# Kernel optimization log

Measured on AMD Instinct MI355X. Metric: run time of the kernel, lower is better.

The kernel has to match this reference:

```python
import jax, jax.numpy as jnp
import numpy as np

FEAT = 256
HID = FEAT // 2
N_KEYS = 2          # output_keys = ["energy_0", "energy_1"]
N_MOLS = 2000
ATOMS_PER_MOL = 100
N_ATOMS = N_MOLS * ATOMS_PER_MOL
LOG2 = 0.6931471805599453


def shifted_softplus(x):
    # NFF's shifted softplus: softplus(x) - log(2)
    return jax.nn.softplus(x) - LOG2


def setup_inputs() -> dict:
    key = jax.random.key(0)
    ks = jax.random.split(key, 6)
    s_i = jax.random.normal(ks[0], (N_ATOMS, FEAT), dtype=jnp.float32)
    xyz = jax.random.normal(ks[1], (N_ATOMS, 3), dtype=jnp.float32)
    num_atoms = jnp.full((N_MOLS,), ATOMS_PER_MOL, dtype=jnp.int64)
    # Per-key MLP params stacked over keys: Linear(F->H), act, Linear(H->1)
    W1 = jax.random.normal(ks[2], (N_KEYS, FEAT, HID), dtype=jnp.float32) / np.sqrt(FEAT)
    b1 = jnp.zeros((N_KEYS, HID), dtype=jnp.float32)
    W2 = jax.random.normal(ks[3], (N_KEYS, HID), dtype=jnp.float32) / np.sqrt(HID)
    b2 = jnp.zeros((N_KEYS,), dtype=jnp.float32)
    return {"s_i": s_i, "xyz": xyz, "num_atoms": num_atoms,
            "W1": W1, "b1": b1, "W2": W2, "b2": b2}


def reference(s_i, xyz, num_atoms, W1, b1, W2, b2):
    n_mols = num_atoms.shape[0]
    # segment id per atom, replacing the torch.split(...)+per-chunk sum loop
    seg = jnp.repeat(jnp.arange(n_mols), num_atoms,
                     total_repeat_length=s_i.shape[0])        # [N]
    # per-key MLP: [K,N,H] hidden, [K,N] scalar output per atom
    h = shifted_softplus(jnp.einsum('nf,kfh->knh', s_i, W1) + b1[:, None, :])
    val = jnp.einsum('knh,kh->kn', h, W2) + b2[:, None]       # [K, N]
    # fused segment-sum pooling -> per-molecule scalars
    pooled = jax.ops.segment_sum(val.T, seg, num_segments=n_mols)  # [M, K]
    return pooled.T                                            # [K, M]
```

## Files before the change

### kernel.cpp

```cpp
#include <hip/hip_runtime.h>

#define FEAT 256
#define HID 128
#define NKEYS 2

typedef __bf16 bf16x8 __attribute__((ext_vector_type(8)));
typedef float f32x16 __attribute__((ext_vector_type(16)));

union Frag {
    bf16x8 v;
    unsigned u[4];
    uint4 q;
};

__device__ __forceinline__ unsigned pack_bf16_2(float f0, float f1) {
    unsigned u0 = __float_as_uint(f0) + 0x8000u;
    unsigned u1 = __float_as_uint(f1) + 0x8000u;
    return __builtin_amdgcn_perm(u1, u0, 0x07060302u);
}

__device__ __forceinline__ float ssp(float x) {
    float sp = __logf(1.0f + __expf(x));
    sp = (x > 15.0f) ? x : sp;
    return sp - 0.69314718056f;
}

__device__ __forceinline__ int find_mol(const int* off, int n_mols, int g) {
    int lo = 0, hi = n_mols;
    while (hi - lo > 1) {
        int mid = (lo + hi) >> 1;
        if (off[mid] <= g) lo = mid; else hi = mid;
    }
    return lo;
}

__device__ __forceinline__ void gload_lds16(const float* g, void* l) {
    __builtin_amdgcn_global_load_lds(
        (const __attribute__((address_space(1))) unsigned int*)g,
        (__attribute__((address_space(3))) unsigned int*)l,
        16, 0, 0);
}

__global__ void prep_kernel(const void* __restrict__ num_atoms_raw,
                            const float* __restrict__ W1,
                            int n_mols, int n_atoms,
                            int* __restrict__ off,
                            unsigned short* __restrict__ Bp,
                            float* __restrict__ out, int out_n) {
    if (blockIdx.x > 0) {
        int idx = (blockIdx.x - 1) * 256 + threadIdx.x;
        int c = idx >> 8;
        int k = idx & 255;
        int key = c >> 7, j = c & 127;
        float f = W1[(size_t)key * FEAT * HID + (size_t)k * HID + j];
        unsigned u = __float_as_uint(f);
        unsigned r = (u + 0x7FFFu + ((u >> 16) & 1u)) >> 16;
        Bp[(size_t)c * FEAT + k] = (unsigned short)r;
        return;
    }
    for (int i = threadIdx.x; i < out_n; i += 256) out[i] = 0.0f;

    __shared__ long long tsum[256];
    __shared__ int csum[256];
    int tid = threadIdx.x;
    const int* a32 = (const int*)num_atoms_raw;
    const long long* a64 = (const long long*)num_atoms_raw;
    int chunk = (n_mols + 255) >> 8;
    int lo = tid * chunk;
    if (lo > n_mols) lo = n_mols;
    int hi = lo + chunk;
    if (hi > n_mols) hi = n_mols;

    long long s32 = 0;
    for (int i = lo; i < hi; ++i) s32 += (long long)a32[i];
    tsum[tid] = s32;
    __syncthreads();
    #pragma unroll
    for (int d = 128; d > 0; d >>= 1) {
        if (tid < d) tsum[tid] += tsum[tid + d];
        __syncthreads();
    }
    int mode = (tsum[0] == (long long)n_atoms) ? 0 : 1;
    long long s = s32;
    if (mode) {
        s = 0;
        for (int i = lo; i < hi; ++i) s += a64[i];
    }
    int v = (int)s;
    csum[tid] = v;
    __syncthreads();
    #pragma unroll
    for (int d = 1; d < 256; d <<= 1) {
        int t = (tid >= d) ? csum[tid - d] : 0;
        __syncthreads();
        csum[tid] += t;
        __syncthreads();
    }
    int run = csum[tid] - v;
    for (int i = lo; i < hi; ++i) {
        off[i] = run;
        run += mode ? (int)a64[i] : a32[i];
    }
    if (hi >= n_mols) off[n_mols] = run;
}

__global__ __launch_bounds__(256, 2)
void gemm_fused(const float* __restrict__ A,
                const unsigned short* __restrict__ Bp,
                const float* __restrict__ b1,
                const float* __restrict__ W2,
                const float* __restrict__ b2,
                const int* __restrict__ off,
                float* __restrict__ out,
                int n_atoms, int n_mols) {
    __shared__ uint4 ldsA[4096];
    int*   offlds = (int*)ldsA;
    float (*part)[64] = (float(*)[64])((char*)ldsA + 8192);
    float (*molacc)[4] = (float(*)[4])((char*)ldsA + 9216);
    int*   mol0sh = (int*)((char*)ldsA + 9248);

    const int tid  = threadIdx.x;
    const int lane = tid & 63;
    const int wid  = tid >> 6;
    const int l31  = lane & 31;
    const int half = lane >> 5;
    const int m0   = blockIdx.x * 64;

    const bool lds_off_ok = (n_mols + 1) <= 2048;
    int4 ov0, ov1;
    if (lds_off_ok) {
        const int4* o4 = (const int4*)off;
        ov0 = o4[tid * 2];
        ov1 = o4[tid * 2 + 1];
    }

    #pragma unroll
    for (int i = 0; i < 4; ++i) {
        const int p   = i * 256 + wid * 64 + lane;
        const int row = p >> 4;
        const int u   = (p & 15) ^ (row & 15);
        int gr = m0 + row;
        if (gr > n_atoms - 1) gr = n_atoms - 1;
        const float* g = A + (size_t)gr * FEAT + u * 4;
        #pragma unroll
        for (int c = 0; c < 4; ++c) {
            gload_lds16(g + c * 64, (void*)&ldsA[c * 1024 + i * 256 + wid * 64]);
        }
    }

    const int c0 = wid * 64 + l31;
    const unsigned short* bb0 = Bp + (size_t)c0 * FEAT + half * 8;
    const unsigned short* bb1 = Bp + (size_t)(c0 + 32) * FEAT + half * 8;
    const int s = l31 & 15;
    const float b1c0 = b1[c0], b1c1 = b1[c0 + 32];
    const float w2c0 = W2[c0], w2c1 = W2[c0 + 32];

    __syncthreads();

    f32x16 acc00 = 0.0f, acc01 = 0.0f, acc10 = 0.0f, acc11 = 0.0f;

    #pragma unroll
    for (int c = 0; c < 4; ++c) {
        const uint4* lbuf = ldsA + c * 1024;
        const int kb = c * 64;
        Frag bf0[4], bf1[4];
        #pragma unroll
        for (int j = 0; j < 4; ++j) {
            bf0[j].q = *(const uint4*)(bb0 + kb + j * 16);
            bf1[j].q = *(const uint4*)(bb1 + kb + j * 16);
        }
        #pragma unroll
        for (int j = 0; j < 4; ++j) {
            const int u0 = j * 4 + half * 2;
            const int q0 = u0 ^ s;
            const int base0 = l31 * 16;
            const int base1 = (l31 + 32) * 16;
            uint4 lo0 = lbuf[base0 + q0];
            uint4 hi0 = lbuf[base0 + (q0 ^ 1)];
            uint4 lo1 = lbuf[base1 + q0];
            uint4 hi1 = lbuf[base1 + (q0 ^ 1)];
            const float4 fl0 = *(const float4*)&lo0;
            const float4 fh0 = *(const float4*)&hi0;
            const float4 fl1 = *(const float4*)&lo1;
            const float4 fh1 = *(const float4*)&hi1;
            Frag a0, a1;
            a0.u[0] = pack_bf16_2(fl0.x, fl0.y);
            a0.u[1] = pack_bf16_2(fl0.z, fl0.w);
            a0.u[2] = pack_bf16_2(fh0.x, fh0.y);
            a0.u[3] = pack_bf16_2(fh0.z, fh0.w);
            a1.u[0] = pack_bf16_2(fl1.x, fl1.y);
            a1.u[1] = pack_bf16_2(fl1.z, fl1.w);
            a1.u[2] = pack_bf16_2(fh1.x, fh1.y);
            a1.u[3] = pack_bf16_2(fh1.z, fh1.w);
            acc00 = __builtin_amdgcn_mfma_f32_32x32x16_bf16(a0.v, bf0[j].v, acc00, 0, 0, 0);
            acc01 = __builtin_amdgcn_mfma_f32_32x32x16_bf16(a0.v, bf1[j].v, acc01, 0, 0, 0);
            acc10 = __builtin_amdgcn_mfma_f32_32x32x16_bf16(a1.v, bf0[j].v, acc10, 0, 0, 0);
            acc11 = __builtin_amdgcn_mfma_f32_32x32x16_bf16(a1.v, bf1[j].v, acc11, 0, 0, 0);
        }
    }

    __syncthreads();

    if (lds_off_ok) {
        ((int4*)offlds)[tid * 2]     = ov0;
        ((int4*)offlds)[tid * 2 + 1] = ov1;
    }
    if (tid < NKEYS * 4) molacc[tid >> 2][tid & 3] = 0.0f;

    #pragma unroll
    for (int rt = 0; rt < 2; ++rt) {
        const f32x16& Ac0 = rt ? acc10 : acc00;
        const f32x16& Ac1 = rt ? acc11 : acc01;
        #pragma unroll
        for (int r = 0; r < 16; ++r) {
            float t = ssp(Ac0[r] + b1c0) * w2c0 + ssp(Ac1[r] + b1c1) * w2c1;
            t += __shfl_xor(t, 1);
            t += __shfl_xor(t, 2);
            t += __shfl_xor(t, 4);
            t += __shfl_xor(t, 8);
            t += __shfl_xor(t, 16);
            if (l31 == r) {
                int row = rt * 32 + (r & 3) + 8 * (r >> 2) + 4 * half;
                part[wid][row] = t;
            }
        }
    }
    __syncthreads();

    if (tid < NKEYS * 64) {
        int key = tid >> 6, r = tid & 63;
        int gm = m0 + r;
        const int* o = lds_off_ok ? offlds : off;
        int mol0 = find_mol(o, n_mols, m0);
        if (tid == 0) *mol0sh = mol0;
        if (gm < n_atoms) {
            int mol = find_mol(o, n_mols, gm);
            float val = part[2 * key][r] + part[2 * key + 1][r] + b2[key];
            int ml = mol - mol0;
            if (ml < 4) atomicAdd(&molacc[key][ml], val);
            else        atomicAdd(&out[(size_t)key * n_mols + mol], val);
        }
    }
    __syncthreads();

    if (tid < NKEYS * 4) {
        int key = tid >> 2, ml = tid & 3;
        int mol = *mol0sh + ml;
        if (mol < n_mols) {
            float v = molacc[key][ml];
            if (v != 0.0f) atomicAdd(&out[(size_t)key * n_mols + mol], v);
        }
    }
}

extern "C" void kernel_launch(void* const* d_in, const int* in_sizes, int n_in,
                              void* d_out, int out_size, void* d_ws, size_t ws_size,
                              hipStream_t stream) {
    const float* s_i      = (const float*)d_in[0];
    const void*  num_atoms = d_in[2];
    const float* W1 = (const float*)d_in[3];
    const float* b1 = (const float*)d_in[4];
    const float* W2 = (const float*)d_in[5];
    const float* b2 = (const float*)d_in[6];
    int n_atoms = in_sizes[0] / FEAT;
    int n_mols  = in_sizes[2];
    float* out = (float*)d_out;

    int* off = (int*)d_ws;
    size_t off_bytes = (((size_t)(n_mols + 1) * 4) + 255) & ~(size_t)255;
    unsigned short* Bp = (unsigned short*)((char*)d_ws + off_bytes);

    int pack_blocks = (NKEYS * HID * FEAT) / 256;
    prep_kernel<<<1 + pack_blocks, 256, 0, stream>>>(num_atoms, W1, n_mols, n_atoms,
                                                     off, Bp, out, out_size);

    int gblocks = (n_atoms + 63) / 64;
    gemm_fused<<<gblocks, 256, 0, stream>>>(s_i, Bp, b1, W2, b2, off, out, n_atoms, n_mols);
}
```

Before: 389.0 us.

## Make fused GEMM persistent with double-buffered LDS staging across tiles

Replaces the one-block-per-64-row-tile launch with a persistent grid of at most 512 blocks of 512 threads. Each block loops over tiles and double-buffers 64-column A chunks in LDS, so the global loads for the next chunk or tile overlap the MFMA work on the current one. Each wave now owns 32 hidden columns instead of 64, which halves the accumulator registers. Molecule lookup and the flush of partial molecule sums are deferred by one tile. In exchange the kernel takes a barrier per K chunk and has more complex cross-tile bookkeeping.

```diff
diff --git a/kernel.cpp b/kernel.cpp
--- a/kernel.cpp
+++ b/kernel.cpp
@@ -104,7 +104,7 @@
     if (hi >= n_mols) off[n_mols] = run;
 }
 
-__global__ __launch_bounds__(256, 2)
+__global__ __launch_bounds__(512, 4)
 void gemm_fused(const float* __restrict__ A,
                 const unsigned short* __restrict__ Bp,
                 const float* __restrict__ b1,
@@ -112,143 +112,165 @@
                 const float* __restrict__ b2,
                 const int* __restrict__ off,
                 float* __restrict__ out,
-                int n_atoms, int n_mols) {
-    __shared__ uint4 ldsA[4096];
-    int*   offlds = (int*)ldsA;
-    float (*part)[64] = (float(*)[64])((char*)ldsA + 8192);
-    float (*molacc)[4] = (float(*)[4])((char*)ldsA + 9216);
-    int*   mol0sh = (int*)((char*)ldsA + 9248);
+                int n_atoms, int n_mols, int ntiles, int stride) {
+    __shared__ uint4  ldsA[2][1024];
+    __shared__ int    offlds[2048];
+    __shared__ float  part[2][8][64];
+    __shared__ int    rowmol[2][64];
+    __shared__ float  molacc[2][NKEYS][4];
 
     const int tid  = threadIdx.x;
     const int lane = tid & 63;
     const int wid  = tid >> 6;
     const int l31  = lane & 31;
     const int half = lane >> 5;
-    const int m0   = blockIdx.x * 64;
-
-    const bool lds_off_ok = (n_mols + 1) <= 2048;
-    int4 ov0, ov1;
-    if (lds_off_ok) {
-        const int4* o4 = (const int4*)off;
-        ov0 = o4[tid * 2];
-        ov1 = o4[tid * 2 + 1];
-    }
-
-    #pragma unroll
-    for (int i = 0; i < 4; ++i) {
-        const int p   = i * 256 + wid * 64 + lane;
-        const int row = p >> 4;
-        const int u   = (p & 15) ^ (row & 15);
-        int gr = m0 + row;
-        if (gr > n_atoms - 1) gr = n_atoms - 1;
-        const float* g = A + (size_t)gr * FEAT + u * 4;
+
+    const bool lds_ok = (n_mols + 1) <= 2048;
+    if (lds_ok) ((int4*)offlds)[tid] = ((const int4*)off)[tid];
+    if (tid < 2 * NKEYS * 4) {
+        int b = tid >> 3;
+        molacc[b][(tid >> 2) & 1][tid & 3] = 0.0f;
+    }
+    const float b2k0 = b2[0], b2k1 = b2[1];
+    const int c0 = wid * 32 + l31;
+    const unsigned short* bb = Bp + (size_t)c0 * FEAT + half * 8;
+    const float b1c = b1[c0];
+    const float w2c = W2[c0];
+    const int rB = l31 + 32;
+    const int x  = l31 & 15;
+
+    int t = blockIdx.x;
+    int cur = 0;
+
+    auto stage = [&](int tile, int c, int buf) {
+        const int m0s = tile * 64;
+        #pragma unroll
+        for (int i = 0; i < 2; ++i) {
+            const int pos = wid * 128 + i * 64;
+            const int r   = (pos >> 4) + (lane >> 4);
+            const int u   = (lane & 15) ^ (r & 15);
+            int gr = m0s + r;
+            if (gr > n_atoms - 1) gr = n_atoms - 1;
+            gload_lds16(A + (size_t)gr * FEAT + c * 64 + u * 4,
+                        (void*)(&ldsA[buf][pos]));
+        }
+    };
+
+    stage(t, 0, 0);
+    __syncthreads();
+
+    int it = 0;
+    for (; t < ntiles; t += stride, ++it) {
+        const int tp = it & 1;
+        const int m0 = t * 64;
+        f32x16 acc0 = 0.0f, acc1 = 0.0f;
+
         #pragma unroll
         for (int c = 0; c < 4; ++c) {
-            gload_lds16(g + c * 64, (void*)&ldsA[c * 1024 + i * 256 + wid * 64]);
+            Frag bw[4];
+            #pragma unroll
+            for (int j = 0; j < 4; ++j)
+                bw[j].q = *(const uint4*)(bb + c * 64 + j * 16);
+            __builtin_amdgcn_sched_barrier(0);
+
+            const bool last = (c == 3) && (t + stride >= ntiles);
+            if (!last) {
+                const int nt = (c < 3) ? t : (t + stride);
+                stage(nt, (c + 1) & 3, cur ^ 1);
+            }
+
+            if (c == 0 && tid < 64) {
+                int gm = m0 + tid;
+                if (gm > n_atoms - 1) gm = n_atoms - 1;
+                rowmol[tp][tid] = lds_ok ? find_mol(offlds, n_mols, gm)
+                                         : find_mol(off, n_mols, gm);
+            }
+
+            const uint4* lbuf = ldsA[cur];
+            #pragma unroll
+            for (int ks = 0; ks < 4; ++ks) {
+                const int u0 = ks * 4 + half * 2;
+                const int us = u0 ^ x;
+                uint4 lo0 = lbuf[l31 * 16 + us];
+                uint4 hi0 = lbuf[l31 * 16 + (us ^ 1)];
+                uint4 lo1 = lbuf[rB  * 16 + us];
+                uint4 hi1 = lbuf[rB  * 16 + (us ^ 1)];
+                const float4 fl0 = *(const float4*)&lo0;
+                const float4 fh0 = *(const float4*)&hi0;
+                const float4 fl1 = *(const float4*)&lo1;
+                const float4 fh1 = *(const float4*)&hi1;
+                Frag a0, a1;
+                a0.u[0] = pack_bf16_2(fl0.x, fl0.y);
+                a0.u[1] = pack_bf16_2(fl0.z, fl0.w);
+                a0.u[2] = pack_bf16_2(fh0.x, fh0.y);
+                a0.u[3] = pack_bf16_2(fh0.z, fh0.w);
+                a1.u[0] = pack_bf16_2(fl1.x, fl1.y);
+                a1.u[1] = pack_bf16_2(fl1.z, fl1.w);
+                a1.u[2] = pack_bf16_2(fh1.x, fh1.y);
+                a1.u[3] = pack_bf16_2(fh1.z, fh1.w);
+                acc0 = __builtin_amdgcn_mfma_f32_32x32x16_bf16(a0.v, bw[ks].v, acc0, 0, 0, 0);
+                acc1 = __builtin_amdgcn_mfma_f32_32x32x16_bf16(a1.v, bw[ks].v, acc1, 0, 0, 0);
+            }
+
+            if (c == 3) {
+                #pragma unroll
+                for (int rt = 0; rt < 2; ++rt) {
+                    const f32x16& Ac = rt ? acc1 : acc0;
+                    #pragma unroll
+                    for (int r = 0; r < 16; ++r) {
+                        float v = ssp(Ac[r] + b1c) * w2c;
+                        v += __shfl_xor(v, 1);
+                        v += __shfl_xor(v, 2);
+                        v += __shfl_xor(v, 4);
+                        v += __shfl_xor(v, 8);
+                        v += __shfl_xor(v, 16);
+                        if (l31 == r) {
+                            int row = rt * 32 + (r & 3) + 8 * (r >> 2) + 4 * half;
+                            part[tp][wid][row] = v;
+                        }
+                    }
+                }
+            }
+
+            __syncthreads();
+            cur ^= 1;
+
+            if (c == 3) {
+                if (it > 0 && tid < NKEYS * 4) {
+                    const int pp = tp ^ 1;
+                    int k = tid >> 2, ml = tid & 3;
+                    int mol = rowmol[pp][0] + ml;
+                    if (mol < n_mols) {
+                        float v = molacc[pp][k][ml];
+                        if (v != 0.0f) atomicAdd(&out[(size_t)k * n_mols + mol], v);
+                        molacc[pp][k][ml] = 0.0f;
+                    }
+                }
+                if (tid < NKEYS * 64) {
+                    int k = tid >> 6, r = tid & 63;
+                    int gm = m0 + r;
+                    if (gm < n_atoms) {
+                        float val = part[tp][4 * k][r] + part[tp][4 * k + 1][r]
+                                  + part[tp][4 * k + 2][r] + part[tp][4 * k + 3][r]
+                                  + (k ? b2k1 : b2k0);
+                        int mol = rowmol[tp][r];
+                        int ml  = mol - rowmol[tp][0];
+                        if (ml < 4) atomicAdd(&molacc[tp][k][ml], val);
+                        else        atomicAdd(&out[(size_t)k * n_mols + mol], val);
+                    }
+                }
+            }
         }
     }
 
-    const int c0 = wid * 64 + l31;
-    const unsigned short* bb0 = Bp + (size_t)c0 * FEAT + half * 8;
-    const unsigned short* bb1 = Bp + (size_t)(c0 + 32) * FEAT + half * 8;
-    const int s = l31 & 15;
-    const float b1c0 = b1[c0], b1c1 = b1[c0 + 32];
-    const float w2c0 = W2[c0], w2c1 = W2[c0 + 32];
-
     __syncthreads();
-
-    f32x16 acc00 = 0.0f, acc01 = 0.0f, acc10 = 0.0f, acc11 = 0.0f;
-
-    #pragma unroll
-    for (int c = 0; c < 4; ++c) {
-        const uint4* lbuf = ldsA + c * 1024;
-        const int kb = c * 64;
-        Frag bf0[4], bf1[4];
-        #pragma unroll
-        for (int j = 0; j < 4; ++j) {
-            bf0[j].q = *(const uint4*)(bb0 + kb + j * 16);
-            bf1[j].q = *(const uint4*)(bb1 + kb + j * 16);
-        }
-        #pragma unroll
-        for (int j = 0; j < 4; ++j) {
-            const int u0 = j * 4 + half * 2;
-            const int q0 = u0 ^ s;
-            const int base0 = l31 * 16;
-            const int base1 = (l31 + 32) * 16;
-            uint4 lo0 = lbuf[base0 + q0];
-            uint4 hi0 = lbuf[base0 + (q0 ^ 1)];
-            uint4 lo1 = lbuf[base1 + q0];
-            uint4 hi1 = lbuf[base1 + (q0 ^ 1)];
-            const float4 fl0 = *(const float4*)&lo0;
-            const float4 fh0 = *(const float4*)&hi0;
-            const float4 fl1 = *(const float4*)&lo1;
-            const float4 fh1 = *(const float4*)&hi1;
-            Frag a0, a1;
-            a0.u[0] = pack_bf16_2(fl0.x, fl0.y);
-            a0.u[1] = pack_bf16_2(fl0.z, fl0.w);
-            a0.u[2] = pack_bf16_2(fh0.x, fh0.y);
-            a0.u[3] = pack_bf16_2(fh0.z, fh0.w);
-            a1.u[0] = pack_bf16_2(fl1.x, fl1.y);
-            a1.u[1] = pack_bf16_2(fl1.z, fl1.w);
-            a1.u[2] = pack_bf16_2(fh1.x, fh1.y);
-            a1.u[3] = pack_bf16_2(fh1.z, fh1.w);
-            acc00 = __builtin_amdgcn_mfma_f32_32x32x16_bf16(a0.v, bf0[j].v, acc00, 0, 0, 0);
-            acc01 = __builtin_amdgcn_mfma_f32_32x32x16_bf16(a0.v, bf1[j].v, acc01, 0, 0, 0);
-            acc10 = __builtin_amdgcn_mfma_f32_32x32x16_bf16(a1.v, bf0[j].v, acc10, 0, 0, 0);
-            acc11 = __builtin_amdgcn_mfma_f32_32x32x16_bf16(a1.v, bf1[j].v, acc11, 0, 0, 0);
-        }
-    }
-
-    __syncthreads();
-
-    if (lds_off_ok) {
-        ((int4*)offlds)[tid * 2]     = ov0;
-        ((int4*)offlds)[tid * 2 + 1] = ov1;
-    }
-    if (tid < NKEYS * 4) molacc[tid >> 2][tid & 3] = 0.0f;
-
-    #pragma unroll
-    for (int rt = 0; rt < 2; ++rt) {
-        const f32x16& Ac0 = rt ? acc10 : acc00;
-        const f32x16& Ac1 = rt ? acc11 : acc01;
-        #pragma unroll
-        for (int r = 0; r < 16; ++r) {
-            float t = ssp(Ac0[r] + b1c0) * w2c0 + ssp(Ac1[r] + b1c1) * w2c1;
-            t += __shfl_xor(t, 1);
-            t += __shfl_xor(t, 2);
-            t += __shfl_xor(t, 4);
-            t += __shfl_xor(t, 8);
-            t += __shfl_xor(t, 16);
-            if (l31 == r) {
-                int row = rt * 32 + (r & 3) + 8 * (r >> 2) + 4 * half;
-                part[wid][row] = t;
-            }
-        }
-    }
-    __syncthreads();
-
-    if (tid < NKEYS * 64) {
-        int key = tid >> 6, r = tid & 63;
-        int gm = m0 + r;
-        const int* o = lds_off_ok ? offlds : off;
-        int mol0 = find_mol(o, n_mols, m0);
-        if (tid == 0) *mol0sh = mol0;
-        if (gm < n_atoms) {
-            int mol = find_mol(o, n_mols, gm);
-            float val = part[2 * key][r] + part[2 * key + 1][r] + b2[key];
-            int ml = mol - mol0;
-            if (ml < 4) atomicAdd(&molacc[key][ml], val);
-            else        atomicAdd(&out[(size_t)key * n_mols + mol], val);
-        }
-    }
-    __syncthreads();
-
+    const int tpl = (it - 1) & 1;
     if (tid < NKEYS * 4) {
-        int key = tid >> 2, ml = tid & 3;
-        int mol = *mol0sh + ml;
+        int k = tid >> 2, ml = tid & 3;
+        int mol = rowmol[tpl][0] + ml;
         if (mol < n_mols) {
-            float v = molacc[key][ml];
-            if (v != 0.0f) atomicAdd(&out[(size_t)key * n_mols + mol], v);
+            float v = molacc[tpl][k][ml];
+            if (v != 0.0f) atomicAdd(&out[(size_t)k * n_mols + mol], v);
         }
     }
 }
@@ -268,12 +290,15 @@
 
     int* off = (int*)d_ws;
     size_t off_bytes = (((size_t)(n_mols + 1) * 4) + 255) & ~(size_t)255;
+    if (off_bytes < 8192) off_bytes = 8192;
     unsigned short* Bp = (unsigned short*)((char*)d_ws + off_bytes);
 
     int pack_blocks = (NKEYS * HID * FEAT) / 256;
     prep_kernel<<<1 + pack_blocks, 256, 0, stream>>>(num_atoms, W1, n_mols, n_atoms,
                                                      off, Bp, out, out_size);
 
-    int gblocks = (n_atoms + 63) / 64;
-    gemm_fused<<<gblocks, 256, 0, stream>>>(s_i, Bp, b1, W2, b2, off, out, n_atoms, n_mols);
-}
+    int ntiles  = (n_atoms + 63) / 64;
+    int nblocks = ntiles < 512 ? ntiles : 512;
+    gemm_fused<<<nblocks, 512, 0, stream>>>(s_i, Bp, b1, W2, b2, off, out,
+                                            n_atoms, n_mols, ntiles, nblocks);
+}
```

Result: faster. 373.0 us (-4.1%).
